# Kernel tuning notes

Measured on AMD Instinct MI355X. Metric: run time of the kernel, lower is better.

## Reference

```python
import jax, jax.numpy as jnp
import numpy as np

N = 12288
E = 393216
IN_DIM = 128
HID = 64
QK = 32
K_HOPS = 2


def setup_inputs() -> dict:
    key = jax.random.key(0)
    ks = jax.random.split(key, 12)
    s = lambda k, shp, fan: jax.random.normal(k, shp, jnp.float32) / np.sqrt(fan)
    return {
        "x_train": jax.random.normal(ks[0], (N, IN_DIM), jnp.float32),
        "x_ori": jax.random.normal(ks[1], (N, IN_DIM), jnp.float32),
        "edge_index": jax.random.randint(ks[2], (2, E), 0, N, jnp.int64),
        "mask": jnp.zeros((N,), jnp.bool_),
        "W1": s(ks[3], (IN_DIM, HID), IN_DIM), "b1": jnp.zeros((HID,), jnp.float32),
        "W2": s(ks[4], (HID, HID), HID),      "b2": jnp.zeros((HID,), jnp.float32),
        "Wq": s(ks[5], (HID, QK), HID),       "bq": jnp.zeros((QK,), jnp.float32),
        "Wk": s(ks[6], (HID, QK), HID),       "bk": jnp.zeros((QK,), jnp.float32),
        "Wv": s(ks[7], (HID, HID), HID),      "bv": jnp.zeros((HID,), jnp.float32),
        "Wdx": s(ks[8], (HID, IN_DIM), HID),  "bdx": jnp.zeros((IN_DIM,), jnp.float32),
    }


def reference(x_train, x_ori, edge_index, mask,
              W1, b1, W2, b2, Wq, bq, Wk, bk, Wv, bv, Wdx, bdx):
    n = x_train.shape[0]
    row, col = edge_index[0], edge_index[1]

    # shared MLP: linear -> relu -> linear2 -> relu
    enc = lambda x: jax.nn.relu(jax.nn.relu(x @ W1 + b1) @ W2 + b2)
    h_ori = enc(x_ori)      # [N, HID]
    h_train = enc(x_train)  # [N, HID]

    # degree of source nodes, D^{-1/2}
    deg = jax.ops.segment_sum(jnp.ones_like(row, jnp.float32), row, num_segments=n)
    d_invsqrt = jnp.clip(deg, 1.0, None) ** -0.5  # [N]
    d_invsqrt = d_invsqrt[:, None]

    def lap(x):
        h = x * d_invsqrt
        out = jax.ops.segment_sum(h[row], col, num_segments=n)
        return x - out * d_invsqrt

    a_feat = 2.0 * h_train - lap(h_train)  # low-pass: 2I - L_sym
    stack = [a_feat]
    x = h_train
    for _ in range(K_HOPS):  # dropout inert in eval mode
        x = lap(x)
        stack.append(x)
    L = jnp.stack(stack, axis=1)  # [N, K+1, HID]

    # attention with global mean-pooled query over h_ori[~mask]
    w = (~mask).astype(jnp.float32)
    q_nodes = h_ori @ Wq + bq                              # [N, QK]
    q_global = (q_nodes * w[:, None]).sum(0) / jnp.clip(w.sum(), 1.0, None)  # [QK]
    keys = L @ Wk + bk   # [N, K+1, QK]
    vals = L @ Wv + bv   # [N, K+1, HID]
    scale = 1.0 / np.sqrt(HID)  # scale uses D = keys feature dim BEFORE projection
    scores = jnp.einsum('q,nkq->nk', q_global, keys) * scale
    A = jax.nn.softmax(scores, axis=-1)          # [N, K+1]
    z = jnp.einsum('nk,nkd->nd', A, vals)        # [N, HID]

    x_hat = z @ Wdx + bdx   # [N, IN_DIM]
    adj_hat = z @ z.T       # [N, N]
    return x_hat, adj_hat
```

## Files before the change

kernel.cpp:

```cpp
#include <hip/hip_runtime.h>
#include <hip/hip_bf16.h>

constexpr int N_  = 12288;
constexpr int E_  = 393216;
constexpr int IND = 128;
constexpr int HID = 64;
constexpr int QKD = 32;
constexpr int CAP = 96;

typedef __attribute__((ext_vector_type(4))) float f4raw;
typedef __attribute__((ext_vector_type(8))) __bf16 bf16x8;
typedef __attribute__((ext_vector_type(4))) __bf16 bf16x4;
typedef __attribute__((ext_vector_type(16))) float f32x16;

__device__ inline bf16x8 lds_read_bf8(const char* base, int row, int k) {
  int off = (row * 128 + k * 2) ^ ((row & 7) << 4);
  uint4 u = *(const uint4*)(base + off);
  union { uint4 u; bf16x8 v; } c; c.u = u; return c.v;
}
__device__ inline void lds_write_bf(char* base, int row, int col, __bf16 v) {
  int off = (row * 128 + col * 2) ^ ((row & 7) << 4);
  *(__bf16*)(base + off) = v;
}

__global__ __launch_bounds__(256) void prep_graph_kernel(
    const float* __restrict__ xo, const float* __restrict__ xt,
    const int* __restrict__ row, const int* __restrict__ col,
    const float* __restrict__ W1, const float* __restrict__ W2,
    const float* __restrict__ Wv, const float* __restrict__ Wdx,
    __bf16* __restrict__ xb, __bf16* __restrict__ W1T, __bf16* __restrict__ W2T,
    __bf16* __restrict__ WvT, __bf16* __restrict__ WdxT,
    int* degRow, int* cntCol, int* __restrict__ csrRow) {
  int b = blockIdx.x, tid = threadIdx.x;
  if (b < 384) {
    int e0 = (b * 256 + tid) * 4;
    int4 r4 = *(const int4*)(row + e0);
    atomicAdd(&degRow[r4.x], 1);
    atomicAdd(&degRow[r4.y], 1);
    atomicAdd(&degRow[r4.z], 1);
    atomicAdd(&degRow[r4.w], 1);
  } else if (b < 768) {
    int e0 = ((b - 384) * 256 + tid) * 4;
    int4 r4 = *(const int4*)(row + e0);
    int4 c4 = *(const int4*)(col + e0);
    int p;
    p = atomicAdd(&cntCol[c4.x], 1); csrRow[c4.x * CAP + p] = r4.x;
    p = atomicAdd(&cntCol[c4.y], 1); csrRow[c4.y * CAP + p] = r4.y;
    p = atomicAdd(&cntCol[c4.z], 1); csrRow[c4.z * CAP + p] = r4.z;
    p = atomicAdd(&cntCol[c4.w], 1); csrRow[c4.w * CAP + p] = r4.w;
  } else if (b < 2304) {
    size_t base = (size_t)(b - 768) * 2048 + (size_t)tid * 8;
    const size_t half = (size_t)N_ * IND;
    const float* src = (base < half) ? (xo + base) : (xt + (base - half));
    f4raw v0 = *(const f4raw*)(src);
    f4raw v1 = *(const f4raw*)(src + 4);
    bf16x8 o;
    o[0] = (__bf16)v0.x; o[1] = (__bf16)v0.y; o[2] = (__bf16)v0.z; o[3] = (__bf16)v0.w;
    o[4] = (__bf16)v1.x; o[5] = (__bf16)v1.y; o[6] = (__bf16)v1.z; o[7] = (__bf16)v1.w;
    *(bf16x8*)(xb + base) = o;
  } else if (b == 2304) {
    for (int e = tid; e < IND * HID; e += 256) {
      int c = e >> 7, k = e & 127;
      W1T[e] = (__bf16)W1[k * HID + c];
    }
  } else if (b == 2305) {
    for (int e = tid; e < HID * HID; e += 256) {
      int c = e >> 6, k = e & 63;
      W2T[e] = (__bf16)W2[k * HID + c];
    }
  } else if (b == 2306) {
    for (int e = tid; e < HID * HID; e += 256) {
      int c = e >> 6, k = e & 63;
      WvT[e] = (__bf16)Wv[k * HID + c];
    }
  } else {
    for (int e = tid; e < HID * IND; e += 256) {
      int c = e >> 6, k = e & 63;
      WdxT[e] = (__bf16)Wdx[k * IND + c];
    }
  }
}

__global__ __launch_bounds__(256) void enc_dinv_kernel(
    const __bf16* __restrict__ xb,
    const __bf16* __restrict__ W1T, const float* __restrict__ b1,
    const __bf16* __restrict__ W2T, const float* __restrict__ b2,
    const int* __restrict__ degRow, const unsigned char* __restrict__ mask,
    float* __restrict__ h_tr, float* __restrict__ dinv, float* __restrict__ gsum) {
  __shared__ __align__(16) char h1s[2][32 * 128];
  __shared__ float wls[64];
  int b = blockIdx.x, tid = threadIdx.x;
  if (b >= 384) {
    int i0 = ((b - 384) * 256 + tid) * 4;
    int4 dg = *(const int4*)(degRow + i0);
    f4raw o = {rsqrtf((float)max(dg.x, 1)), rsqrtf((float)max(dg.y, 1)),
               rsqrtf((float)max(dg.z, 1)), rsqrtf((float)max(dg.w, 1))};
    *(f4raw*)(dinv + i0) = o;
    return;
  }
  bool ori = b < 192;
  int row0 = (ori ? b : b - 192) * 64;
  const __bf16* xrow = xb + (ori ? (size_t)0 : (size_t)N_ * IND) + (size_t)row0 * IND;
  if (ori && tid < 64) wls[tid] = mask[row0 + tid] ? 0.f : 1.f;
  int wave = tid >> 6, lane = tid & 63;
  int p = wave >> 1, w2 = wave & 1;
  int lr = lane & 31, hi = lane >> 5;
  int colc = w2 * 32 + lr;
  f32x16 acc = (f32x16)(0.f);
  const __bf16* wcol = W1T + (size_t)colc * IND + hi * 8;
  const __bf16* arow = xrow + (size_t)(p * 32 + lr) * IND + hi * 8;
#pragma unroll
  for (int kk = 0; kk < 8; ++kk) {
    bf16x8 a = *(const bf16x8*)(arow + kk * 16);
    bf16x8 bq = *(const bf16x8*)(wcol + kk * 16);
    acc = __builtin_amdgcn_mfma_f32_32x32x16_bf16(a, bq, acc, 0, 0, 0);
  }
  float b1l = b1[colc];
#pragma unroll
  for (int reg = 0; reg < 16; ++reg) {
    int rr = (reg & 3) + 8 * (reg >> 2) + 4 * hi;
    float v = fmaxf(acc[reg] + b1l, 0.f);
    lds_write_bf(h1s[p], rr, colc, (__bf16)v);
  }
  __syncthreads();
  f32x16 acc2 = (f32x16)(0.f);
  const __bf16* wcol2 = W2T + (size_t)colc * HID + hi * 8;
#pragma unroll
  for (int kk = 0; kk < 4; ++kk) {
    bf16x8 a = lds_read_bf8(h1s[p], lr, kk * 16 + hi * 8);
    bf16x8 bq = *(const bf16x8*)(wcol2 + kk * 16);
    acc2 = __builtin_amdgcn_mfma_f32_32x32x16_bf16(a, bq, acc2, 0, 0, 0);
  }
  float b2l = b2[colc];
  if (ori) {
    float part = 0.f;
#pragma unroll
    for (int reg = 0; reg < 16; ++reg) {
      int rr = (reg & 3) + 8 * (reg >> 2) + 4 * hi;
      float v = fmaxf(acc2[reg] + b2l, 0.f);
      part = fmaf(wls[p * 32 + rr], v, part);
    }
    atomicAdd(&gsum[colc], part);
    if (tid == 0) {
      float wl = 0.f;
      for (int r = 0; r < 64; ++r) wl += wls[r];
      atomicAdd(&gsum[64], wl);
    }
  } else {
#pragma unroll
    for (int reg = 0; reg < 16; ++reg) {
      int rr = (reg & 3) + 8 * (reg >> 2) + 4 * hi;
      float v = fmaxf(acc2[reg] + b2l, 0.f);
      h_tr[(size_t)(row0 + p * 32 + rr) * HID + colc] = v;
    }
  }
}

__global__ __launch_bounds__(256) void lap1_kernel(
    const float* __restrict__ h, const float* __restrict__ dinv,
    const int* __restrict__ cnt, const int* __restrict__ csrRow,
    float* __restrict__ lap1d) {
  int lane = threadIdx.x & 63, wv = threadIdx.x >> 6;
  int g = lane >> 4, t = lane & 15;
  int c = blockIdx.x * 16 + wv * 4 + g;
  int s0 = c * CAP, s1 = s0 + cnt[c];
  f4raw a0 = (f4raw)(0.f), a1 = (f4raw)(0.f), a2 = (f4raw)(0.f), a3 = (f4raw)(0.f);
  int i = s0;
  for (; i + 3 < s1; i += 4) {
    int r0 = csrRow[i], r1 = csrRow[i + 1], r2 = csrRow[i + 2], r3 = csrRow[i + 3];
    a0 += (*(const f4raw*)(h + (size_t)r0 * HID + t * 4)) * dinv[r0];
    a1 += (*(const f4raw*)(h + (size_t)r1 * HID + t * 4)) * dinv[r1];
    a2 += (*(const f4raw*)(h + (size_t)r2 * HID + t * 4)) * dinv[r2];
    a3 += (*(const f4raw*)(h + (size_t)r3 * HID + t * 4)) * dinv[r3];
  }
  for (; i < s1; ++i) {
    int r0 = csrRow[i];
    a0 += (*(const f4raw*)(h + (size_t)r0 * HID + t * 4)) * dinv[r0];
  }
  float d = dinv[c];
  size_t idx = (size_t)c * HID + t * 4;
  f4raw hc = *(const f4raw*)(h + idx);
  *(f4raw*)(lap1d + idx) = (hc - ((a0 + a1) + (a2 + a3)) * d) * d;
}

__global__ __launch_bounds__(256) void lap2_attnz_xhat_kernel(
    const float* __restrict__ h, const float* __restrict__ lap1d,
    const float* __restrict__ dinv,
    const int* __restrict__ cnt, const int* __restrict__ csrRow,
    const float* __restrict__ gsum,
    const float* __restrict__ Wq, const float* __restrict__ bq,
    const float* __restrict__ Wk, const float* __restrict__ bk,
    const __bf16* __restrict__ WvT, const float* __restrict__ bv,
    const __bf16* __restrict__ WdxT, const float* __restrict__ bdx,
    float* __restrict__ xhat, __bf16* __restrict__ zb) {
  __shared__ float l2s[32][68];
  __shared__ __align__(16) char zps[32 * 128];
  __shared__ __align__(16) char zsl[32 * 128];
  __shared__ float qg[QKD];
  __shared__ float kqs[72];
  int tid = threadIdx.x;
  int row0 = blockIdx.x * 32;
  float wsum = gsum[64];
  if (tid < QKD) {
    float inv = 1.0f / fmaxf(wsum, 1.0f);
    float a = bq[tid] * wsum;
    for (int d0 = 0; d0 < HID; ++d0) a = fmaf(gsum[d0], Wq[d0 * QKD + tid], a);
    qg[tid] = a * inv;
  }
  int grp = tid >> 4, t = tid & 15;
#pragma unroll
  for (int it = 0; it < 2; ++it) {
    int r = grp + 16 * it;
    int c = row0 + r;
    int s0 = c * CAP, s1 = s0 + cnt[c];
    f4raw a0 = (f4raw)(0.f), a1 = (f4raw)(0.f), a2 = (f4raw)(0.f), a3 = (f4raw)(0.f);
    int i = s0;
    for (; i + 3 < s1; i += 4) {
      int r0 = csrRow[i], r1 = csrRow[i + 1], r2 = csrRow[i + 2], r3 = csrRow[i + 3];
      a0 += *(const f4raw*)(lap1d + (size_t)r0 * HID + t * 4);
      a1 += *(const f4raw*)(lap1d + (size_t)r1 * HID + t * 4);
      a2 += *(const f4raw*)(lap1d + (size_t)r2 * HID + t * 4);
      a3 += *(const f4raw*)(lap1d + (size_t)r3 * HID + t * 4);
    }
    for (; i < s1; ++i) {
      int r0 = csrRow[i];
      a0 += *(const f4raw*)(lap1d + (size_t)r0 * HID + t * 4);
    }
    float d = dinv[c];
    float rd = 1.0f / d;
    f4raw lv = *(const f4raw*)(lap1d + (size_t)c * HID + t * 4);
    *(f4raw*)&l2s[r][t * 4] = lv * rd - ((a0 + a1) + (a2 + a3)) * d;
  }
  __syncthreads();
  if (tid < 64) {
    float a = 0.f;
    for (int q = 0; q < QKD; ++q) a = fmaf(Wk[tid * QKD + q], qg[q], a);
    kqs[tid] = a * 0.125f;
  } else if (tid == 64) {
    float sb = 0.f;
    for (int q = 0; q < QKD; ++q) sb = fmaf(bk[q], qg[q], sb);
    kqs[64] = sb * 0.125f;
  }
  __syncthreads();
  f4raw kq4 = *(const f4raw*)(&kqs[t * 4]);
  float sbias = kqs[64];
#pragma unroll
  for (int it = 0; it < 2; ++it) {
    int r = grp + 16 * it;
    int c = row0 + r;
    size_t idx = (size_t)c * HID + t * 4;
    float d = dinv[c];
    float rd = 1.0f / d;
    f4raw hv = *(const f4raw*)(h + idx);
    f4raw v1 = *(const f4raw*)(lap1d + idx) * rd;
    f4raw v2 = *(const f4raw*)&l2s[r][t * 4];
    f4raw av = 2.f * hv - v1;
    float s0 = av.x * kq4.x + av.y * kq4.y + av.z * kq4.z + av.w * kq4.w;
    float s1 = v1.x * kq4.x + v1.y * kq4.y + v1.z * kq4.z + v1.w * kq4.w;
    float s2 = v2.x * kq4.x + v2.y * kq4.y + v2.z * kq4.z + v2.w * kq4.w;
#pragma unroll
    for (int o = 1; o < 16; o <<= 1) {
      s0 += __shfl_xor(s0, o);
      s1 += __shfl_xor(s1, o);
      s2 += __shfl_xor(s2, o);
    }
    s0 += sbias; s1 += sbias; s2 += sbias;
    float m = fmaxf(s0, fmaxf(s1, s2));
    float e0 = __expf(s0 - m), e1 = __expf(s1 - m), e2 = __expf(s2 - m);
    float is = 1.f / (e0 + e1 + e2);
    f4raw zp = (e0 * av + e1 * v1 + e2 * v2) * is;
    bf16x4 z4;
    z4[0] = (__bf16)zp.x; z4[1] = (__bf16)zp.y; z4[2] = (__bf16)zp.z; z4[3] = (__bf16)zp.w;
    int off = (r * 128 + t * 8) ^ ((r & 7) << 4);
    *(bf16x4*)(zps + off) = z4;
  }
  __syncthreads();
  int wave = tid >> 6, lane = tid & 63;
  int lr = lane & 31, hi = lane >> 5;
  if (wave < 2) {
    int col = wave * 32 + lr;
    f32x16 accz = (f32x16)(0.f);
    const __bf16* wv = WvT + (size_t)col * HID + hi * 8;
#pragma unroll
    for (int kk = 0; kk < 4; ++kk) {
      bf16x8 a = lds_read_bf8(zps, lr, kk * 16 + hi * 8);
      bf16x8 bq = *(const bf16x8*)(wv + kk * 16);
      accz = __builtin_amdgcn_mfma_f32_32x32x16_bf16(a, bq, accz, 0, 0, 0);
    }
    float bvl = bv[col];
#pragma unroll
    for (int reg = 0; reg < 16; ++reg) {
      int rr = (reg & 3) + 8 * (reg >> 2) + 4 * hi;
      __bf16 vb = (__bf16)(accz[reg] + bvl);
      zb[(size_t)(row0 + rr) * HID + col] = vb;
      lds_write_bf(zsl, rr, col, vb);
    }
  }
  __syncthreads();
  {
    int c0 = wave * 32 + lr;
    f32x16 acx = (f32x16)(0.f);
    const __bf16* wd = WdxT + (size_t)c0 * HID + hi * 8;
#pragma unroll
    for (int kk = 0; kk < 4; ++kk) {
      bf16x8 a = lds_read_bf8(zsl, lr, kk * 16 + hi * 8);
      bf16x8 bq = *(const bf16x8*)(wd + kk * 16);
      acx = __builtin_amdgcn_mfma_f32_32x32x16_bf16(a, bq, acx, 0, 0, 0);
    }
    float bdl = bdx[c0];
#pragma unroll
    for (int reg = 0; reg < 16; ++reg) {
      int rr = (reg & 3) + 8 * (reg >> 2) + 4 * hi;
      xhat[(size_t)(row0 + rr) * IND + c0] = acx[reg] + bdl;
    }
  }
}

__global__ __launch_bounds__(256) void adj_mfma_kernel(
    const __bf16* __restrict__ z, float* __restrict__ out) {
  int tid = threadIdx.x;
  int wave = tid >> 6, lane = tid & 63;
  int wr = wave >> 1, wc = wave & 1;
  int rb = blockIdx.y, cb = blockIdx.x;
  int lr = lane & 31, hi = lane >> 5;

  size_t arow0 = (size_t)(rb * 128 + wr * 64 + lr) * HID;
  size_t arow1 = arow0 + (size_t)32 * HID;
  size_t brow0 = (size_t)(cb * 128 + wc * 64 + lr) * HID;
  size_t brow1 = brow0 + (size_t)32 * HID;
  int kbase = hi * 8;

  f32x16 acc00 = (f32x16)(0.f), acc01 = (f32x16)(0.f);
  f32x16 acc10 = (f32x16)(0.f), acc11 = (f32x16)(0.f);

#pragma unroll
  for (int kk = 0; kk < 4; ++kk) {
    int k0 = kk * 16 + kbase;
    bf16x8 a0 = *(const bf16x8*)(z + arow0 + k0);
    bf16x8 a1 = *(const bf16x8*)(z + arow1 + k0);
    bf16x8 b0 = *(const bf16x8*)(z + brow0 + k0);
    bf16x8 b1 = *(const bf16x8*)(z + brow1 + k0);
    acc00 = __builtin_amdgcn_mfma_f32_32x32x16_bf16(a0, b0, acc00, 0, 0, 0);
    acc01 = __builtin_amdgcn_mfma_f32_32x32x16_bf16(a0, b1, acc01, 0, 0, 0);
    acc10 = __builtin_amdgcn_mfma_f32_32x32x16_bf16(a1, b0, acc10, 0, 0, 0);
    acc11 = __builtin_amdgcn_mfma_f32_32x32x16_bf16(a1, b1, acc11, 0, 0, 0);
  }

  int colb = cb * 128 + wc * 64 + lr;
  int rowb = rb * 128 + wr * 64 + 4 * hi;
#pragma unroll
  for (int reg = 0; reg < 16; ++reg) {
    int rr = (reg & 3) + 8 * (reg >> 2);
    size_t r0 = (size_t)(rowb + rr);
    __builtin_nontemporal_store(acc00[reg], out + r0 * N_ + colb);
    __builtin_nontemporal_store(acc01[reg], out + r0 * N_ + colb + 32);
    __builtin_nontemporal_store(acc10[reg], out + (r0 + 32) * N_ + colb);
    __builtin_nontemporal_store(acc11[reg], out + (r0 + 32) * N_ + colb + 32);
  }
}

extern "C" void kernel_launch(void* const* d_in, const int* in_sizes, int n_in,
                              void* d_out, int out_size, void* d_ws, size_t ws_size,
                              hipStream_t stream) {
  const float* x_train = (const float*)d_in[0];
  const float* x_ori   = (const float*)d_in[1];
  const int*   ei      = (const int*)d_in[2];
  const unsigned char* mask = (const unsigned char*)d_in[3];
  const float* W1  = (const float*)d_in[4];
  const float* b1  = (const float*)d_in[5];
  const float* W2  = (const float*)d_in[6];
  const float* b2  = (const float*)d_in[7];
  const float* Wq  = (const float*)d_in[8];
  const float* bq  = (const float*)d_in[9];
  const float* Wk  = (const float*)d_in[10];
  const float* bk  = (const float*)d_in[11];
  const float* Wv  = (const float*)d_in[12];
  const float* bv  = (const float*)d_in[13];
  const float* Wdx = (const float*)d_in[14];
  const float* bdx = (const float*)d_in[15];

  char* ws = (char*)d_ws;
  size_t o = 0;
  auto alloc = [&](size_t bytes) -> void* {
    void* p = ws + o;
    o += (bytes + 255) & ~(size_t)255;
    return p;
  };
  __bf16* xb    = (__bf16*)alloc((size_t)2 * N_ * IND * 2);
  __bf16* W1T   = (__bf16*)alloc((size_t)IND * HID * 2);
  __bf16* W2T   = (__bf16*)alloc((size_t)HID * HID * 2);
  __bf16* WvT   = (__bf16*)alloc((size_t)HID * HID * 2);
  __bf16* WdxT  = (__bf16*)alloc((size_t)HID * IND * 2);
  float* h_tr   = (float*)alloc((size_t)N_ * HID * 4);
  float* lap1d  = (float*)alloc((size_t)N_ * HID * 4);
  __bf16* zb    = (__bf16*)alloc((size_t)N_ * HID * 2);
  float* dinv   = (float*)alloc((size_t)N_ * 4);
  int*   csrRow = (int*)alloc((size_t)N_ * CAP * 4);
  int*   zero0  = (int*)alloc((size_t)(2 * N_ + 65) * 4);
  int*   degRow = zero0;
  int*   cntCol = zero0 + N_;
  float* gsum   = (float*)(zero0 + 2 * N_);

  const int* row = ei;
  const int* col = ei + E_;

  (void)hipMemsetAsync(zero0, 0, (size_t)(2 * N_ + 65) * 4, stream);

  prep_graph_kernel<<<2308, 256, 0, stream>>>(x_ori, x_train, row, col,
                                              W1, W2, Wv, Wdx,
                                              xb, W1T, W2T, WvT, WdxT,
                                              degRow, cntCol, csrRow);
  enc_dinv_kernel<<<396, 256, 0, stream>>>(xb, W1T, b1, W2T, b2, degRow, mask,
                                           h_tr, dinv, gsum);
  lap1_kernel<<<N_ / 16, 256, 0, stream>>>(h_tr, dinv, cntCol, csrRow, lap1d);

  float* outp = (float*)d_out;
  lap2_attnz_xhat_kernel<<<N_ / 32, 256, 0, stream>>>(h_tr, lap1d, dinv,
                                                      cntCol, csrRow, gsum,
                                                      Wq, bq, Wk, bk, WvT, bv,
                                                      WdxT, bdx, outp, zb);
  adj_mfma_kernel<<<dim3(96, 96), 256, 0, stream>>>(zb, outp + (size_t)N_ * IND);
}
```

Baseline: 248.3 us.

## Fuse pre-adjacency stages into one persistent kernel with grid barriers

Replaces four separate launches (graph prep, encoder, first Laplacian, second Laplacian with attention and x_hat) with a single persistent kernel of 256 blocks of 512 threads. Each block holds two 256-thread sub-units that loop over the old work items, and stages are separated by atomic-counter grid barriers. This removes kernel launch and drain gaps between the small stages. In exchange it gives up parallelism in stages that had more blocks than the 512 sub-units. It also relies on all 256 blocks being co-resident, otherwise the barriers deadlock.

```diff
diff --git a/kernel.cpp b/kernel.cpp
--- a/kernel.cpp
+++ b/kernel.cpp
@@ -7,6 +7,7 @@
 constexpr int HID = 64;
 constexpr int QKD = 32;
 constexpr int CAP = 96;
+constexpr int NBLK = 256;
 
 typedef __attribute__((ext_vector_type(4))) float f4raw;
 typedef __attribute__((ext_vector_type(8))) __bf16 bf16x8;
@@ -23,295 +24,320 @@
   *(__bf16*)(base + off) = v;
 }
 
-__global__ __launch_bounds__(256) void prep_graph_kernel(
+__device__ __forceinline__ void gbar(int* bar, int gen) {
+  __syncthreads();
+  if (threadIdx.x == 0) {
+    __threadfence();
+    int v = __hip_atomic_fetch_add(&bar[gen - 1], 1, __ATOMIC_ACQ_REL, __HIP_MEMORY_SCOPE_AGENT);
+    if (v == NBLK - 1) {
+      __hip_atomic_store(&bar[3], gen, __ATOMIC_RELEASE, __HIP_MEMORY_SCOPE_AGENT);
+    } else {
+      while (__hip_atomic_load(&bar[3], __ATOMIC_ACQUIRE, __HIP_MEMORY_SCOPE_AGENT) < gen) {
+        __builtin_amdgcn_s_sleep(2);
+      }
+    }
+  }
+  __syncthreads();
+}
+
+__global__ __launch_bounds__(512, 2) void mega_kernel(
     const float* __restrict__ xo, const float* __restrict__ xt,
     const int* __restrict__ row, const int* __restrict__ col,
-    const float* __restrict__ W1, const float* __restrict__ W2,
-    const float* __restrict__ Wv, const float* __restrict__ Wdx,
+    const float* __restrict__ W1, const float* __restrict__ b1,
+    const float* __restrict__ W2, const float* __restrict__ b2,
+    const float* __restrict__ Wq, const float* __restrict__ bq,
+    const float* __restrict__ Wk, const float* __restrict__ bk,
+    const float* __restrict__ Wv, const float* __restrict__ bv,
+    const float* __restrict__ Wdx, const float* __restrict__ bdx,
+    const unsigned char* __restrict__ mask,
     __bf16* __restrict__ xb, __bf16* __restrict__ W1T, __bf16* __restrict__ W2T,
     __bf16* __restrict__ WvT, __bf16* __restrict__ WdxT,
-    int* degRow, int* cntCol, int* __restrict__ csrRow) {
-  int b = blockIdx.x, tid = threadIdx.x;
-  if (b < 384) {
-    int e0 = (b * 256 + tid) * 4;
-    int4 r4 = *(const int4*)(row + e0);
-    atomicAdd(&degRow[r4.x], 1);
-    atomicAdd(&degRow[r4.y], 1);
-    atomicAdd(&degRow[r4.z], 1);
-    atomicAdd(&degRow[r4.w], 1);
-  } else if (b < 768) {
-    int e0 = ((b - 384) * 256 + tid) * 4;
-    int4 r4 = *(const int4*)(row + e0);
-    int4 c4 = *(const int4*)(col + e0);
-    int p;
-    p = atomicAdd(&cntCol[c4.x], 1); csrRow[c4.x * CAP + p] = r4.x;
-    p = atomicAdd(&cntCol[c4.y], 1); csrRow[c4.y * CAP + p] = r4.y;
-    p = atomicAdd(&cntCol[c4.z], 1); csrRow[c4.z * CAP + p] = r4.z;
-    p = atomicAdd(&cntCol[c4.w], 1); csrRow[c4.w * CAP + p] = r4.w;
-  } else if (b < 2304) {
-    size_t base = (size_t)(b - 768) * 2048 + (size_t)tid * 8;
-    const size_t half = (size_t)N_ * IND;
-    const float* src = (base < half) ? (xo + base) : (xt + (base - half));
-    f4raw v0 = *(const f4raw*)(src);
-    f4raw v1 = *(const f4raw*)(src + 4);
-    bf16x8 o;
-    o[0] = (__bf16)v0.x; o[1] = (__bf16)v0.y; o[2] = (__bf16)v0.z; o[3] = (__bf16)v0.w;
-    o[4] = (__bf16)v1.x; o[5] = (__bf16)v1.y; o[6] = (__bf16)v1.z; o[7] = (__bf16)v1.w;
-    *(bf16x8*)(xb + base) = o;
-  } else if (b == 2304) {
-    for (int e = tid; e < IND * HID; e += 256) {
-      int c = e >> 7, k = e & 127;
-      W1T[e] = (__bf16)W1[k * HID + c];
-    }
-  } else if (b == 2305) {
-    for (int e = tid; e < HID * HID; e += 256) {
-      int c = e >> 6, k = e & 63;
-      W2T[e] = (__bf16)W2[k * HID + c];
-    }
-  } else if (b == 2306) {
-    for (int e = tid; e < HID * HID; e += 256) {
-      int c = e >> 6, k = e & 63;
-      WvT[e] = (__bf16)Wv[k * HID + c];
-    }
-  } else {
-    for (int e = tid; e < HID * IND; e += 256) {
-      int c = e >> 6, k = e & 63;
-      WdxT[e] = (__bf16)Wdx[k * IND + c];
-    }
-  }
-}
-
-__global__ __launch_bounds__(256) void enc_dinv_kernel(
-    const __bf16* __restrict__ xb,
-    const __bf16* __restrict__ W1T, const float* __restrict__ b1,
-    const __bf16* __restrict__ W2T, const float* __restrict__ b2,
-    const int* __restrict__ degRow, const unsigned char* __restrict__ mask,
-    float* __restrict__ h_tr, float* __restrict__ dinv, float* __restrict__ gsum) {
-  __shared__ __align__(16) char h1s[2][32 * 128];
-  __shared__ float wls[64];
-  int b = blockIdx.x, tid = threadIdx.x;
-  if (b >= 384) {
-    int i0 = ((b - 384) * 256 + tid) * 4;
-    int4 dg = *(const int4*)(degRow + i0);
-    f4raw o = {rsqrtf((float)max(dg.x, 1)), rsqrtf((float)max(dg.y, 1)),
-               rsqrtf((float)max(dg.z, 1)), rsqrtf((float)max(dg.w, 1))};
-    *(f4raw*)(dinv + i0) = o;
-    return;
-  }
-  bool ori = b < 192;
-  int row0 = (ori ? b : b - 192) * 64;
-  const __bf16* xrow = xb + (ori ? (size_t)0 : (size_t)N_ * IND) + (size_t)row0 * IND;
-  if (ori && tid < 64) wls[tid] = mask[row0 + tid] ? 0.f : 1.f;
-  int wave = tid >> 6, lane = tid & 63;
-  int p = wave >> 1, w2 = wave & 1;
-  int lr = lane & 31, hi = lane >> 5;
-  int colc = w2 * 32 + lr;
-  f32x16 acc = (f32x16)(0.f);
-  const __bf16* wcol = W1T + (size_t)colc * IND + hi * 8;
-  const __bf16* arow = xrow + (size_t)(p * 32 + lr) * IND + hi * 8;
-#pragma unroll
-  for (int kk = 0; kk < 8; ++kk) {
-    bf16x8 a = *(const bf16x8*)(arow + kk * 16);
-    bf16x8 bq = *(const bf16x8*)(wcol + kk * 16);
-    acc = __builtin_amdgcn_mfma_f32_32x32x16_bf16(a, bq, acc, 0, 0, 0);
-  }
-  float b1l = b1[colc];
-#pragma unroll
-  for (int reg = 0; reg < 16; ++reg) {
-    int rr = (reg & 3) + 8 * (reg >> 2) + 4 * hi;
-    float v = fmaxf(acc[reg] + b1l, 0.f);
-    lds_write_bf(h1s[p], rr, colc, (__bf16)v);
-  }
-  __syncthreads();
-  f32x16 acc2 = (f32x16)(0.f);
-  const __bf16* wcol2 = W2T + (size_t)colc * HID + hi * 8;
-#pragma unroll
-  for (int kk = 0; kk < 4; ++kk) {
-    bf16x8 a = lds_read_bf8(h1s[p], lr, kk * 16 + hi * 8);
-    bf16x8 bq = *(const bf16x8*)(wcol2 + kk * 16);
-    acc2 = __builtin_amdgcn_mfma_f32_32x32x16_bf16(a, bq, acc2, 0, 0, 0);
-  }
-  float b2l = b2[colc];
-  if (ori) {
-    float part = 0.f;
-#pragma unroll
-    for (int reg = 0; reg < 16; ++reg) {
-      int rr = (reg & 3) + 8 * (reg >> 2) + 4 * hi;
-      float v = fmaxf(acc2[reg] + b2l, 0.f);
-      part = fmaf(wls[p * 32 + rr], v, part);
-    }
-    atomicAdd(&gsum[colc], part);
-    if (tid == 0) {
-      float wl = 0.f;
-      for (int r = 0; r < 64; ++r) wl += wls[r];
-      atomicAdd(&gsum[64], wl);
-    }
-  } else {
-#pragma unroll
-    for (int reg = 0; reg < 16; ++reg) {
-      int rr = (reg & 3) + 8 * (reg >> 2) + 4 * hi;
-      float v = fmaxf(acc2[reg] + b2l, 0.f);
-      h_tr[(size_t)(row0 + p * 32 + rr) * HID + colc] = v;
-    }
-  }
-}
-
-__global__ __launch_bounds__(256) void lap1_kernel(
-    const float* __restrict__ h, const float* __restrict__ dinv,
-    const int* __restrict__ cnt, const int* __restrict__ csrRow,
-    float* __restrict__ lap1d) {
-  int lane = threadIdx.x & 63, wv = threadIdx.x >> 6;
-  int g = lane >> 4, t = lane & 15;
-  int c = blockIdx.x * 16 + wv * 4 + g;
-  int s0 = c * CAP, s1 = s0 + cnt[c];
-  f4raw a0 = (f4raw)(0.f), a1 = (f4raw)(0.f), a2 = (f4raw)(0.f), a3 = (f4raw)(0.f);
-  int i = s0;
-  for (; i + 3 < s1; i += 4) {
-    int r0 = csrRow[i], r1 = csrRow[i + 1], r2 = csrRow[i + 2], r3 = csrRow[i + 3];
-    a0 += (*(const f4raw*)(h + (size_t)r0 * HID + t * 4)) * dinv[r0];
-    a1 += (*(const f4raw*)(h + (size_t)r1 * HID + t * 4)) * dinv[r1];
-    a2 += (*(const f4raw*)(h + (size_t)r2 * HID + t * 4)) * dinv[r2];
-    a3 += (*(const f4raw*)(h + (size_t)r3 * HID + t * 4)) * dinv[r3];
-  }
-  for (; i < s1; ++i) {
-    int r0 = csrRow[i];
-    a0 += (*(const f4raw*)(h + (size_t)r0 * HID + t * 4)) * dinv[r0];
-  }
-  float d = dinv[c];
-  size_t idx = (size_t)c * HID + t * 4;
-  f4raw hc = *(const f4raw*)(h + idx);
-  *(f4raw*)(lap1d + idx) = (hc - ((a0 + a1) + (a2 + a3)) * d) * d;
-}
-
-__global__ __launch_bounds__(256) void lap2_attnz_xhat_kernel(
-    const float* __restrict__ h, const float* __restrict__ lap1d,
-    const float* __restrict__ dinv,
-    const int* __restrict__ cnt, const int* __restrict__ csrRow,
-    const float* __restrict__ gsum,
-    const float* __restrict__ Wq, const float* __restrict__ bq,
-    const float* __restrict__ Wk, const float* __restrict__ bk,
-    const __bf16* __restrict__ WvT, const float* __restrict__ bv,
-    const __bf16* __restrict__ WdxT, const float* __restrict__ bdx,
-    float* __restrict__ xhat, __bf16* __restrict__ zb) {
-  __shared__ float l2s[32][68];
-  __shared__ __align__(16) char zps[32 * 128];
-  __shared__ __align__(16) char zsl[32 * 128];
-  __shared__ float qg[QKD];
-  __shared__ float kqs[72];
+    float* __restrict__ h_tr, float* __restrict__ dinv, float* __restrict__ lap1d,
+    float* __restrict__ xhat, __bf16* __restrict__ zb,
+    int* degRow, int* cntCol, int* __restrict__ csrRow, float* gsum, int* bar) {
+  __shared__ __align__(16) char smem[2][17408];
   int tid = threadIdx.x;
-  int row0 = blockIdx.x * 32;
-  float wsum = gsum[64];
-  if (tid < QKD) {
-    float inv = 1.0f / fmaxf(wsum, 1.0f);
-    float a = bq[tid] * wsum;
-    for (int d0 = 0; d0 < HID; ++d0) a = fmaf(gsum[d0], Wq[d0 * QKD + tid], a);
-    qg[tid] = a * inv;
-  }
-  int grp = tid >> 4, t = tid & 15;
-#pragma unroll
-  for (int it = 0; it < 2; ++it) {
-    int r = grp + 16 * it;
-    int c = row0 + r;
-    int s0 = c * CAP, s1 = s0 + cnt[c];
+  int u = tid >> 8, utid = tid & 255;
+  int uid = (int)blockIdx.x * 2 + u;
+  char* sm = smem[u];
+
+  for (int w = uid; w < 2308; w += 512) {
+    if (w < 384) {
+      int e0 = (w * 256 + utid) * 4;
+      int4 r4 = *(const int4*)(row + e0);
+      atomicAdd(&degRow[r4.x], 1);
+      atomicAdd(&degRow[r4.y], 1);
+      atomicAdd(&degRow[r4.z], 1);
+      atomicAdd(&degRow[r4.w], 1);
+    } else if (w < 768) {
+      int e0 = ((w - 384) * 256 + utid) * 4;
+      int4 r4 = *(const int4*)(row + e0);
+      int4 c4 = *(const int4*)(col + e0);
+      int p;
+      p = atomicAdd(&cntCol[c4.x], 1); csrRow[c4.x * CAP + p] = r4.x;
+      p = atomicAdd(&cntCol[c4.y], 1); csrRow[c4.y * CAP + p] = r4.y;
+      p = atomicAdd(&cntCol[c4.z], 1); csrRow[c4.z * CAP + p] = r4.z;
+      p = atomicAdd(&cntCol[c4.w], 1); csrRow[c4.w * CAP + p] = r4.w;
+    } else if (w < 2304) {
+      size_t base = (size_t)(w - 768) * 2048 + (size_t)utid * 8;
+      const size_t half = (size_t)N_ * IND;
+      const float* src = (base < half) ? (xo + base) : (xt + (base - half));
+      f4raw v0 = *(const f4raw*)(src);
+      f4raw v1 = *(const f4raw*)(src + 4);
+      bf16x8 o;
+      o[0] = (__bf16)v0.x; o[1] = (__bf16)v0.y; o[2] = (__bf16)v0.z; o[3] = (__bf16)v0.w;
+      o[4] = (__bf16)v1.x; o[5] = (__bf16)v1.y; o[6] = (__bf16)v1.z; o[7] = (__bf16)v1.w;
+      *(bf16x8*)(xb + base) = o;
+    } else if (w == 2304) {
+      for (int e = utid; e < IND * HID; e += 256) {
+        int c = e >> 7, k = e & 127;
+        W1T[e] = (__bf16)W1[k * HID + c];
+      }
+    } else if (w == 2305) {
+      for (int e = utid; e < HID * HID; e += 256) {
+        int c = e >> 6, k = e & 63;
+        W2T[e] = (__bf16)W2[k * HID + c];
+      }
+    } else if (w == 2306) {
+      for (int e = utid; e < HID * HID; e += 256) {
+        int c = e >> 6, k = e & 63;
+        WvT[e] = (__bf16)Wv[k * HID + c];
+      }
+    } else {
+      for (int e = utid; e < HID * IND; e += 256) {
+        int c = e >> 6, k = e & 63;
+        WdxT[e] = (__bf16)Wdx[k * IND + c];
+      }
+    }
+  }
+  gbar(bar, 1);
+
+  {
+    const int w = uid;
+    const bool act = w < 396;
+    const bool isenc = act && (w < 384);
+    if (act && !isenc) {
+      int i0 = ((w - 384) * 256 + utid) * 4;
+      int4 dg = *(const int4*)(degRow + i0);
+      f4raw o = {rsqrtf((float)max(dg.x, 1)), rsqrtf((float)max(dg.y, 1)),
+                 rsqrtf((float)max(dg.z, 1)), rsqrtf((float)max(dg.w, 1))};
+      *(f4raw*)(dinv + i0) = o;
+    }
+    const bool ori = w < 192;
+    const int row0 = (ori ? w : w - 192) * 64;
+    float* wls = (float*)(sm + 8192);
+    if (isenc && ori && utid < 64) wls[utid] = mask[row0 + utid] ? 0.f : 1.f;
+    int wave = utid >> 6, lane = utid & 63;
+    int p = wave >> 1, w2 = wave & 1;
+    int lr = lane & 31, hi = lane >> 5;
+    int colc = w2 * 32 + lr;
+    char* h1p = sm + p * 4096;
+    if (isenc) {
+      const __bf16* xrow = xb + (ori ? (size_t)0 : (size_t)N_ * IND) + (size_t)row0 * IND;
+      f32x16 acc = (f32x16)(0.f);
+      const __bf16* wcol = W1T + (size_t)colc * IND + hi * 8;
+      const __bf16* arow = xrow + (size_t)(p * 32 + lr) * IND + hi * 8;
+#pragma unroll
+      for (int kk = 0; kk < 8; ++kk) {
+        bf16x8 a = *(const bf16x8*)(arow + kk * 16);
+        bf16x8 bq = *(const bf16x8*)(wcol + kk * 16);
+        acc = __builtin_amdgcn_mfma_f32_32x32x16_bf16(a, bq, acc, 0, 0, 0);
+      }
+      float b1l = b1[colc];
+#pragma unroll
+      for (int reg = 0; reg < 16; ++reg) {
+        int rr = (reg & 3) + 8 * (reg >> 2) + 4 * hi;
+        lds_write_bf(h1p, rr, colc, (__bf16)fmaxf(acc[reg] + b1l, 0.f));
+      }
+    }
+    __syncthreads();
+    if (isenc) {
+      f32x16 acc2 = (f32x16)(0.f);
+      const __bf16* wcol2 = W2T + (size_t)colc * HID + hi * 8;
+#pragma unroll
+      for (int kk = 0; kk < 4; ++kk) {
+        bf16x8 a = lds_read_bf8(h1p, lr, kk * 16 + hi * 8);
+        bf16x8 bq = *(const bf16x8*)(wcol2 + kk * 16);
+        acc2 = __builtin_amdgcn_mfma_f32_32x32x16_bf16(a, bq, acc2, 0, 0, 0);
+      }
+      float b2l = b2[colc];
+      if (ori) {
+        float part = 0.f;
+#pragma unroll
+        for (int reg = 0; reg < 16; ++reg) {
+          int rr = (reg & 3) + 8 * (reg >> 2) + 4 * hi;
+          part = fmaf(wls[p * 32 + rr], fmaxf(acc2[reg] + b2l, 0.f), part);
+        }
+        atomicAdd(&gsum[colc], part);
+        if (utid == 0) {
+          float wl = 0.f;
+          for (int r = 0; r < 64; ++r) wl += wls[r];
+          atomicAdd(&gsum[64], wl);
+        }
+      } else {
+#pragma unroll
+        for (int reg = 0; reg < 16; ++reg) {
+          int rr = (reg & 3) + 8 * (reg >> 2) + 4 * hi;
+          h_tr[(size_t)(row0 + p * 32 + rr) * HID + colc] = fmaxf(acc2[reg] + b2l, 0.f);
+        }
+      }
+    }
+  }
+  gbar(bar, 2);
+
+  for (int w = uid; w < 768; w += 512) {
+    int lane = utid & 63, wv = utid >> 6;
+    int g = lane >> 4, t = lane & 15;
+    int c = w * 16 + wv * 4 + g;
+    int s0 = c * CAP, s1 = s0 + cntCol[c];
     f4raw a0 = (f4raw)(0.f), a1 = (f4raw)(0.f), a2 = (f4raw)(0.f), a3 = (f4raw)(0.f);
     int i = s0;
     for (; i + 3 < s1; i += 4) {
       int r0 = csrRow[i], r1 = csrRow[i + 1], r2 = csrRow[i + 2], r3 = csrRow[i + 3];
-      a0 += *(const f4raw*)(lap1d + (size_t)r0 * HID + t * 4);
-      a1 += *(const f4raw*)(lap1d + (size_t)r1 * HID + t * 4);
-      a2 += *(const f4raw*)(lap1d + (size_t)r2 * HID + t * 4);
-      a3 += *(const f4raw*)(lap1d + (size_t)r3 * HID + t * 4);
+      a0 += (*(const f4raw*)(h_tr + (size_t)r0 * HID + t * 4)) * dinv[r0];
+      a1 += (*(const f4raw*)(h_tr + (size_t)r1 * HID + t * 4)) * dinv[r1];
+      a2 += (*(const f4raw*)(h_tr + (size_t)r2 * HID + t * 4)) * dinv[r2];
+      a3 += (*(const f4raw*)(h_tr + (size_t)r3 * HID + t * 4)) * dinv[r3];
     }
     for (; i < s1; ++i) {
       int r0 = csrRow[i];
-      a0 += *(const f4raw*)(lap1d + (size_t)r0 * HID + t * 4);
+      a0 += (*(const f4raw*)(h_tr + (size_t)r0 * HID + t * 4)) * dinv[r0];
     }
     float d = dinv[c];
-    float rd = 1.0f / d;
-    f4raw lv = *(const f4raw*)(lap1d + (size_t)c * HID + t * 4);
-    *(f4raw*)&l2s[r][t * 4] = lv * rd - ((a0 + a1) + (a2 + a3)) * d;
-  }
-  __syncthreads();
-  if (tid < 64) {
-    float a = 0.f;
-    for (int q = 0; q < QKD; ++q) a = fmaf(Wk[tid * QKD + q], qg[q], a);
-    kqs[tid] = a * 0.125f;
-  } else if (tid == 64) {
-    float sb = 0.f;
-    for (int q = 0; q < QKD; ++q) sb = fmaf(bk[q], qg[q], sb);
-    kqs[64] = sb * 0.125f;
-  }
-  __syncthreads();
-  f4raw kq4 = *(const f4raw*)(&kqs[t * 4]);
-  float sbias = kqs[64];
-#pragma unroll
-  for (int it = 0; it < 2; ++it) {
-    int r = grp + 16 * it;
-    int c = row0 + r;
     size_t idx = (size_t)c * HID + t * 4;
-    float d = dinv[c];
-    float rd = 1.0f / d;
-    f4raw hv = *(const f4raw*)(h + idx);
-    f4raw v1 = *(const f4raw*)(lap1d + idx) * rd;
-    f4raw v2 = *(const f4raw*)&l2s[r][t * 4];
-    f4raw av = 2.f * hv - v1;
-    float s0 = av.x * kq4.x + av.y * kq4.y + av.z * kq4.z + av.w * kq4.w;
-    float s1 = v1.x * kq4.x + v1.y * kq4.y + v1.z * kq4.z + v1.w * kq4.w;
-    float s2 = v2.x * kq4.x + v2.y * kq4.y + v2.z * kq4.z + v2.w * kq4.w;
-#pragma unroll
-    for (int o = 1; o < 16; o <<= 1) {
-      s0 += __shfl_xor(s0, o);
-      s1 += __shfl_xor(s1, o);
-      s2 += __shfl_xor(s2, o);
-    }
-    s0 += sbias; s1 += sbias; s2 += sbias;
-    float m = fmaxf(s0, fmaxf(s1, s2));
-    float e0 = __expf(s0 - m), e1 = __expf(s1 - m), e2 = __expf(s2 - m);
-    float is = 1.f / (e0 + e1 + e2);
-    f4raw zp = (e0 * av + e1 * v1 + e2 * v2) * is;
-    bf16x4 z4;
-    z4[0] = (__bf16)zp.x; z4[1] = (__bf16)zp.y; z4[2] = (__bf16)zp.z; z4[3] = (__bf16)zp.w;
-    int off = (r * 128 + t * 8) ^ ((r & 7) << 4);
-    *(bf16x4*)(zps + off) = z4;
-  }
-  __syncthreads();
-  int wave = tid >> 6, lane = tid & 63;
-  int lr = lane & 31, hi = lane >> 5;
-  if (wave < 2) {
-    int col = wave * 32 + lr;
-    f32x16 accz = (f32x16)(0.f);
-    const __bf16* wv = WvT + (size_t)col * HID + hi * 8;
-#pragma unroll
-    for (int kk = 0; kk < 4; ++kk) {
-      bf16x8 a = lds_read_bf8(zps, lr, kk * 16 + hi * 8);
-      bf16x8 bq = *(const bf16x8*)(wv + kk * 16);
-      accz = __builtin_amdgcn_mfma_f32_32x32x16_bf16(a, bq, accz, 0, 0, 0);
-    }
-    float bvl = bv[col];
-#pragma unroll
-    for (int reg = 0; reg < 16; ++reg) {
-      int rr = (reg & 3) + 8 * (reg >> 2) + 4 * hi;
-      __bf16 vb = (__bf16)(accz[reg] + bvl);
-      zb[(size_t)(row0 + rr) * HID + col] = vb;
-      lds_write_bf(zsl, rr, col, vb);
-    }
-  }
-  __syncthreads();
+    f4raw hc = *(const f4raw*)(h_tr + idx);
+    *(f4raw*)(lap1d + idx) = (hc - ((a0 + a1) + (a2 + a3)) * d) * d;
+  }
+  gbar(bar, 3);
+
   {
-    int c0 = wave * 32 + lr;
-    f32x16 acx = (f32x16)(0.f);
-    const __bf16* wd = WdxT + (size_t)c0 * HID + hi * 8;
-#pragma unroll
-    for (int kk = 0; kk < 4; ++kk) {
-      bf16x8 a = lds_read_bf8(zsl, lr, kk * 16 + hi * 8);
-      bf16x8 bq = *(const bf16x8*)(wd + kk * 16);
-      acx = __builtin_amdgcn_mfma_f32_32x32x16_bf16(a, bq, acx, 0, 0, 0);
-    }
-    float bdl = bdx[c0];
-#pragma unroll
-    for (int reg = 0; reg < 16; ++reg) {
-      int rr = (reg & 3) + 8 * (reg >> 2) + 4 * hi;
-      xhat[(size_t)(row0 + rr) * IND + c0] = acx[reg] + bdl;
+    const int w = uid;
+    const bool act = w < 384;
+    const int row0 = w * 32;
+    float (*l2s)[68] = (float(*)[68])sm;
+    char* zps = sm + 8704;
+    char* zsl = sm + 12800;
+    float* qg  = (float*)(sm + 16896);
+    float* kqs = (float*)(sm + 17024);
+    float wsum = gsum[64];
+    if (act && utid < QKD) {
+      float inv = 1.0f / fmaxf(wsum, 1.0f);
+      float a = bq[utid] * wsum;
+      for (int d0 = 0; d0 < HID; ++d0) a = fmaf(gsum[d0], Wq[d0 * QKD + utid], a);
+      qg[utid] = a * inv;
+    }
+    int grp = utid >> 4, t = utid & 15;
+    if (act) {
+#pragma unroll
+      for (int it = 0; it < 2; ++it) {
+        int r = grp + 16 * it;
+        int c = row0 + r;
+        int s0 = c * CAP, s1 = s0 + cntCol[c];
+        f4raw a0 = (f4raw)(0.f), a1 = (f4raw)(0.f), a2 = (f4raw)(0.f), a3 = (f4raw)(0.f);
+        int i = s0;
+        for (; i + 3 < s1; i += 4) {
+          int r0 = csrRow[i], r1 = csrRow[i + 1], r2 = csrRow[i + 2], r3 = csrRow[i + 3];
+          a0 += *(const f4raw*)(lap1d + (size_t)r0 * HID + t * 4);
+          a1 += *(const f4raw*)(lap1d + (size_t)r1 * HID + t * 4);
+          a2 += *(const f4raw*)(lap1d + (size_t)r2 * HID + t * 4);
+          a3 += *(const f4raw*)(lap1d + (size_t)r3 * HID + t * 4);
+        }
+        for (; i < s1; ++i) {
+          int r0 = csrRow[i];
+          a0 += *(const f4raw*)(lap1d + (size_t)r0 * HID + t * 4);
+        }
+        float d = dinv[c];
+        float rd = 1.0f / d;
+        f4raw lv = *(const f4raw*)(lap1d + (size_t)c * HID + t * 4);
+        *(f4raw*)&l2s[r][t * 4] = lv * rd - ((a0 + a1) + (a2 + a3)) * d;
+      }
+    }
+    __syncthreads();
+    if (act) {
+      if (utid < 64) {
+        float a = 0.f;
+        for (int q = 0; q < QKD; ++q) a = fmaf(Wk[utid * QKD + q], qg[q], a);
+        kqs[utid] = a * 0.125f;
+      } else if (utid == 64) {
+        float sb = 0.f;
+        for (int q = 0; q < QKD; ++q) sb = fmaf(bk[q], qg[q], sb);
+        kqs[64] = sb * 0.125f;
+      }
+    }
+    __syncthreads();
+    if (act) {
+      f4raw kq4 = *(const f4raw*)(&kqs[t * 4]);
+      float sbias = kqs[64];
+#pragma unroll
+      for (int it = 0; it < 2; ++it) {
+        int r = grp + 16 * it;
+        int c = row0 + r;
+        size_t idx = (size_t)c * HID + t * 4;
+        float d = dinv[c];
+        float rd = 1.0f / d;
+        f4raw hv = *(const f4raw*)(h_tr + idx);
+        f4raw v1 = *(const f4raw*)(lap1d + idx) * rd;
+        f4raw v2 = *(const f4raw*)&l2s[r][t * 4];
+        f4raw av = 2.f * hv - v1;
+        float s0 = av.x * kq4.x + av.y * kq4.y + av.z * kq4.z + av.w * kq4.w;
+        float s1 = v1.x * kq4.x + v1.y * kq4.y + v1.z * kq4.z + v1.w * kq4.w;
+        float s2 = v2.x * kq4.x + v2.y * kq4.y + v2.z * kq4.z + v2.w * kq4.w;
+#pragma unroll
+        for (int o = 1; o < 16; o <<= 1) {
+          s0 += __shfl_xor(s0, o);
+          s1 += __shfl_xor(s1, o);
+          s2 += __shfl_xor(s2, o);
+        }
+        s0 += sbias; s1 += sbias; s2 += sbias;
+        float m = fmaxf(s0, fmaxf(s1, s2));
+        float e0 = __expf(s0 - m), e1 = __expf(s1 - m), e2 = __expf(s2 - m);
+        float is = 1.f / (e0 + e1 + e2);
+        f4raw zp = (e0 * av + e1 * v1 + e2 * v2) * is;
+        bf16x4 z4;
+        z4[0] = (__bf16)zp.x; z4[1] = (__bf16)zp.y; z4[2] = (__bf16)zp.z; z4[3] = (__bf16)zp.w;
+        int off = (r * 128 + t * 8) ^ ((r & 7) << 4);
+        *(bf16x4*)(zps + off) = z4;
+      }
+    }
+    __syncthreads();
+    int wave = utid >> 6, lane = utid & 63;
+    int lr = lane & 31, hi = lane >> 5;
+    if (act && wave < 2) {
+      int colz = wave * 32 + lr;
+      f32x16 accz = (f32x16)(0.f);
+      const __bf16* wv = WvT + (size_t)colz * HID + hi * 8;
+#pragma unroll
+      for (int kk = 0; kk < 4; ++kk) {
+        bf16x8 a = lds_read_bf8(zps, lr, kk * 16 + hi * 8);
+        bf16x8 bq = *(const bf16x8*)(wv + kk * 16);
+        accz = __builtin_amdgcn_mfma_f32_32x32x16_bf16(a, bq, accz, 0, 0, 0);
+      }
+      float bvl = bv[colz];
+#pragma unroll
+      for (int reg = 0; reg < 16; ++reg) {
+        int rr = (reg & 3) + 8 * (reg >> 2) + 4 * hi;
+        __bf16 vb = (__bf16)(accz[reg] + bvl);
+        zb[(size_t)(row0 + rr) * HID + colz] = vb;
+        lds_write_bf(zsl, rr, colz, vb);
+      }
+    }
+    __syncthreads();
+    if (act) {
+      int c0 = wave * 32 + lr;
+      f32x16 acx = (f32x16)(0.f);
+      const __bf16* wd = WdxT + (size_t)c0 * HID + hi * 8;
+#pragma unroll
+      for (int kk = 0; kk < 4; ++kk) {
+        bf16x8 a = lds_read_bf8(zsl, lr, kk * 16 + hi * 8);
+        bf16x8 bq = *(const bf16x8*)(wd + kk * 16);
+        acx = __builtin_amdgcn_mfma_f32_32x32x16_bf16(a, bq, acx, 0, 0, 0);
+      }
+      float bdl = bdx[c0];
+#pragma unroll
+      for (int reg = 0; reg < 16; ++reg) {
+        int rr = (reg & 3) + 8 * (reg >> 2) + 4 * hi;
+        xhat[(size_t)(row0 + rr) * IND + c0] = acx[reg] + bdl;
+      }
     }
   }
 }
@@ -396,28 +422,23 @@
   __bf16* zb    = (__bf16*)alloc((size_t)N_ * HID * 2);
   float* dinv   = (float*)alloc((size_t)N_ * 4);
   int*   csrRow = (int*)alloc((size_t)N_ * CAP * 4);
-  int*   zero0  = (int*)alloc((size_t)(2 * N_ + 65) * 4);
+  int*   zero0  = (int*)alloc((size_t)(2 * N_ + 65 + 8) * 4);
   int*   degRow = zero0;
   int*   cntCol = zero0 + N_;
   float* gsum   = (float*)(zero0 + 2 * N_);
+  int*   bar    = zero0 + 2 * N_ + 65;
 
   const int* row = ei;
   const int* col = ei + E_;
 
-  (void)hipMemsetAsync(zero0, 0, (size_t)(2 * N_ + 65) * 4, stream);
-
-  prep_graph_kernel<<<2308, 256, 0, stream>>>(x_ori, x_train, row, col,
-                                              W1, W2, Wv, Wdx,
-                                              xb, W1T, W2T, WvT, WdxT,
-                                              degRow, cntCol, csrRow);
-  enc_dinv_kernel<<<396, 256, 0, stream>>>(xb, W1T, b1, W2T, b2, degRow, mask,
-                                           h_tr, dinv, gsum);
-  lap1_kernel<<<N_ / 16, 256, 0, stream>>>(h_tr, dinv, cntCol, csrRow, lap1d);
+  (void)hipMemsetAsync(zero0, 0, (size_t)(2 * N_ + 65 + 8) * 4, stream);
 
   float* outp = (float*)d_out;
-  lap2_attnz_xhat_kernel<<<N_ / 32, 256, 0, stream>>>(h_tr, lap1d, dinv,
-                                                      cntCol, csrRow, gsum,
-                                                      Wq, bq, Wk, bk, WvT, bv,
-                                                      WdxT, bdx, outp, zb);
+  mega_kernel<<<NBLK, 512, 0, stream>>>(x_ori, x_train, row, col,
+                                        W1, b1, W2, b2, Wq, bq, Wk, bk,
+                                        Wv, bv, Wdx, bdx, mask,
+                                        xb, W1T, W2T, WvT, WdxT,
+                                        h_tr, dinv, lap1d, outp, zb,
+                                        degRow, cntCol, csrRow, gsum, bar);
   adj_mfma_kernel<<<dim3(96, 96), 256, 0, stream>>>(zb, outp + (size_t)N_ * IND);
 }
```

Measured after the change: 373.7 us. +50.5%, slower.
